# Kernel tuning notes

Hardware: AMD Instinct MI355X
Metric: run time of the kernel (lower is better)

The kernel has to match this reference:

```python
import jax, jax.numpy as jnp
import numpy as np

BETA = 0.01  # soft-threshold level (init kwarg)
EPS = 1e-12


def vector_to_toeplitz(v):
    # v: [2N-1] complex generator; T[i, j] = v[N-1 + i - j], shape [N, N]
    n = (v.shape[0] + 1) // 2
    ii = jnp.arange(n)[:, None]
    jj = jnp.arange(n)[None, :]
    return v[(n - 1) + ii - jj]


def soft_thresh(z, beta):
    # complex soft-threshold (proximal op of beta*||.||_1):
    # z * max(|z| - beta, 0) / |z|
    mag = jnp.abs(z)
    scale = jnp.maximum(mag - beta, 0.0) / jnp.maximum(mag, EPS)
    return z * scale.astype(z.real.dtype)


def setup_inputs() -> dict:
    key = jax.random.key(0)
    ks = jax.random.split(key, 8)
    N, M, B = 1024, 256, 1024
    d = jnp.float32
    return {
        "v_re": jax.random.normal(ks[0], (2 * N - 1,), d),
        "v_im": jax.random.normal(ks[1], (2 * N - 1,), d),
        "W2_re": jax.random.normal(ks[2], (N, M), d) / np.sqrt(M),
        "W2_im": jax.random.normal(ks[3], (N, M), d) / np.sqrt(M),
        "x_re": jax.random.normal(ks[4], (N, B), d),
        "x_im": jax.random.normal(ks[5], (N, B), d),
        "y_re": jax.random.normal(ks[6], (M, B), d),
        "y_im": jax.random.normal(ks[7], (M, B), d),
    }


def reference(v_re, v_im, W2_re, W2_im, x_re, x_im, y_re, y_im):
    v = jax.lax.complex(v_re, v_im)      # [2N-1]
    W2 = jax.lax.complex(W2_re, W2_im)   # [N, M] (= A^H)
    x = jax.lax.complex(x_re, x_im)      # [N, B]
    y = jax.lax.complex(y_re, y_im)      # [M, B]
    W1 = vector_to_toeplitz(v)           # [N, N] Toeplitz
    # tpm(W1, x) + W2 @ y, then complex soft-threshold
    z = soft_thresh(W1 @ x + W2 @ y, BETA)  # [N, B]
    return z
```

## Files before the change

kernel.cpp:

```cpp
#include <hip/hip_runtime.h>
#include <hip/hip_fp16.h>
#include <cstdint>
#include <cstddef>


#define K_DIM 2560
#define BETA_F 0.01f
#define EPS_F  1e-12f

typedef __attribute__((ext_vector_type(8))) _Float16 half8;
typedef __attribute__((ext_vector_type(4))) _Float16 half4;
typedef __attribute__((ext_vector_type(4))) float   floatx4;

__device__ alignas(16) _Float16 g_Ap[1024 * K_DIM];
__device__ alignas(16) _Float16 g_Bt[2048 * K_DIM];
__device__ alignas(16) float    g_P[4][1024 * 2048];

__global__ __launch_bounds__(256) void build_all(
    const float* __restrict__ v_re, const float* __restrict__ v_im,
    const float* __restrict__ W2_re, const float* __restrict__ W2_im,
    const float* __restrict__ x_re, const float* __restrict__ x_im,
    const float* __restrict__ y_re, const float* __restrict__ y_im)
{
    const int bx = blockIdx.x;
    if (bx < 1280) {
        int t = bx * 256 + threadIdx.x;
        int i  = t / 320;
        int c  = t - i * 320;
        int kp = c * 8;
        half8 h;
        if (kp < 1024) {
#pragma unroll
            for (int j = 0; j < 8; ++j) h[j] = (_Float16)v_re[1023 + i - kp - j];
        } else if (kp < 1280) {
            const float* s = W2_re + i * 256 + (kp - 1024);
#pragma unroll
            for (int j = 0; j < 8; ++j) h[j] = (_Float16)s[j];
        } else if (kp < 2304) {
            int k2 = kp - 1280;
#pragma unroll
            for (int j = 0; j < 8; ++j) h[j] = (_Float16)v_im[1023 + i - k2 - j];
        } else {
            const float* s = W2_im + i * 256 + (kp - 2304);
#pragma unroll
            for (int j = 0; j < 8; ++j) h[j] = (_Float16)s[j];
        }
        *reinterpret_cast<half8*>(g_Ap + (size_t)i * K_DIM + kp) = h;
        return;
    }
    __shared__ float lre[32][33];
    __shared__ float lim[32][33];
    int idx = bx - 1280;
    int bk  = idx % 40;
    int by  = idx / 40;
    const float* sre = (bk < 32) ? x_re : y_re;
    const float* sim = (bk < 32) ? x_im : y_im;
    int kb   = (bk < 32) ? bk : (bk - 32);
    int koff = (bk < 32) ? 0 : 1024;
    int k0 = kb * 32;
    int n0 = by * 32;
    int tid = threadIdx.x;
    int tx = tid & 31, ty = tid >> 5;
#pragma unroll
    for (int s = 0; s < 4; ++s) {
        int kk = ty + 8 * s;
        lre[kk][tx] = sre[(size_t)(k0 + kk) * 1024 + n0 + tx];
        lim[kk][tx] = sim[(size_t)(k0 + kk) * 1024 + n0 + tx];
    }
    __syncthreads();
    int lane_n = tid >> 3;
    int kq     = (tid & 7) * 4;
    half4 hre, him, hmim;
#pragma unroll
    for (int j = 0; j < 4; ++j) {
        float re = lre[kq + j][lane_n];
        float im = lim[kq + j][lane_n];
        hre[j]  = (_Float16)re;
        him[j]  = (_Float16)im;
        hmim[j] = (_Float16)(-im);
    }
    int n = n0 + lane_n;
    size_t kk2 = (size_t)koff + k0 + kq;
    _Float16* r0 = g_Bt + (size_t)(2 * n)     * K_DIM;
    _Float16* r1 = g_Bt + (size_t)(2 * n + 1) * K_DIM;
    *reinterpret_cast<half4*>(r0 + kk2)        = hre;
    *reinterpret_cast<half4*>(r0 + kk2 + 1280) = hmim;
    *reinterpret_cast<half4*>(r1 + kk2)        = him;
    *reinterpret_cast<half4*>(r1 + kk2 + 1280) = hre;
}

__global__ __launch_bounds__(256, 8) void gemm_split(void)
{
    __shared__ __align__(16) _Float16 As[2 * 2 * 64 * 32];
    __shared__ __align__(16) _Float16 Bs[2 * 2 * 64 * 32];

    const int tid  = threadIdx.x;
    const int lane = tid & 63;
    const int w    = tid >> 6;
    const int wm   = w >> 1;
    const int wn   = w & 1;

    const int bid   = blockIdx.x;
    const int xcd   = bid & 7;
    const int t     = bid >> 3;
    const int split = t & 3;
    const int tile  = t >> 2;
    const int mi0 = ((xcd & 1) * 8 + (tile & 7)) * 64;
    const int ni0 = ((xcd >> 1) * 8 + (tile >> 3)) * 64;
    const int ks  = split * 640;
    float* __restrict__ P = g_P[split];

    floatx4 acc[2][2];
#pragma unroll
    for (int a = 0; a < 2; ++a)
#pragma unroll
        for (int b = 0; b < 2; ++b) acc[a][b] = (floatx4)0.0f;

    const int rS = tid >> 2;
    const int jS = tid & 3;
    const int s0 = ((rS & 15) >> 1) & 3;
    char* asW = (char*)As + rS * 64 + ((jS ^ s0) * 16);
    char* bsW = (char*)Bs + rS * 64 + ((jS ^ s0) * 16);
    const _Float16* gA = g_Ap + (size_t)(mi0 + rS) * K_DIM + ks + jS * 8;
    const _Float16* gB = g_Bt + (size_t)(ni0 + rS) * K_DIM + ks + jS * 8;

    const int rowA = lane & 15;
    const int q    = lane >> 4;
    const int coff = (q ^ ((rowA >> 1) & 3)) * 16;

    {
        half8 pA0 = *reinterpret_cast<const half8*>(gA);
        half8 pA1 = *reinterpret_cast<const half8*>(gA + 32);
        half8 pB0 = *reinterpret_cast<const half8*>(gB);
        half8 pB1 = *reinterpret_cast<const half8*>(gB + 32);
        *reinterpret_cast<half8*>(asW)        = pA0;
        *reinterpret_cast<half8*>(asW + 4096) = pA1;
        *reinterpret_cast<half8*>(bsW)        = pB0;
        *reinterpret_cast<half8*>(bsW + 4096) = pB1;
    }
    __syncthreads();

    const int NIT = 640 / 64;
    for (int kt = 0; kt < NIT; ++kt) {
        const int cur = kt & 1;
        half8 pA0, pA1, pB0, pB1;
        if (kt < NIT - 1) {
            const _Float16* ga = gA + (kt + 1) * 64;
            const _Float16* gb = gB + (kt + 1) * 64;
            pA0 = *reinterpret_cast<const half8*>(ga);
            pA1 = *reinterpret_cast<const half8*>(ga + 32);
            pB0 = *reinterpret_cast<const half8*>(gb);
            pB1 = *reinterpret_cast<const half8*>(gb + 32);
        }
        const char* Ab = (const char*)As + cur * 8192;
        const char* Bb = (const char*)Bs + cur * 8192;
        half8 af[2][2], bf[2][2];
#pragma unroll
        for (int mi = 0; mi < 2; ++mi) {
            int r = wm * 32 + mi * 16 + rowA;
            af[mi][0] = *reinterpret_cast<const half8*>(Ab + r * 64 + coff);
            af[mi][1] = *reinterpret_cast<const half8*>(Ab + 4096 + r * 64 + coff);
        }
#pragma unroll
        for (int ni = 0; ni < 2; ++ni) {
            int r = wn * 32 + ni * 16 + rowA;
            bf[ni][0] = *reinterpret_cast<const half8*>(Bb + r * 64 + coff);
            bf[ni][1] = *reinterpret_cast<const half8*>(Bb + 4096 + r * 64 + coff);
        }
#pragma unroll
        for (int mi = 0; mi < 2; ++mi)
#pragma unroll
            for (int ni = 0; ni < 2; ++ni) {
                acc[mi][ni] = __builtin_amdgcn_mfma_f32_16x16x32_f16(
                    af[mi][0], bf[ni][0], acc[mi][ni], 0, 0, 0);
                acc[mi][ni] = __builtin_amdgcn_mfma_f32_16x16x32_f16(
                    af[mi][1], bf[ni][1], acc[mi][ni], 0, 0, 0);
            }
        if (kt < NIT - 1) {
            char* aw = asW + (cur ^ 1) * 8192;
            char* bw = bsW + (cur ^ 1) * 8192;
            *reinterpret_cast<half8*>(aw)        = pA0;
            *reinterpret_cast<half8*>(aw + 4096) = pA1;
            *reinterpret_cast<half8*>(bw)        = pB0;
            *reinterpret_cast<half8*>(bw + 4096) = pB1;
        }
        __syncthreads();
    }

    const int colL  = lane & 15;
    const int rquad = (lane >> 4) * 4;
#pragma unroll
    for (int mi = 0; mi < 2; ++mi)
#pragma unroll
        for (int ni = 0; ni < 2; ++ni)
#pragma unroll
            for (int r = 0; r < 4; ++r) {
                int row = mi0 + wm * 32 + mi * 16 + rquad + r;
                int col = ni0 + wn * 32 + ni * 16 + colL;
                P[(size_t)row * 2048 + col] = acc[mi][ni][r];
            }
}

__global__ __launch_bounds__(256) void reduce_soft(float* __restrict__ out,
                                                   int out_n)
{
    int t = blockIdx.x * 256 + threadIdx.x;
    floatx4 v0 = reinterpret_cast<const floatx4*>(g_P[0])[t];
    floatx4 v1 = reinterpret_cast<const floatx4*>(g_P[1])[t];
    floatx4 v2 = reinterpret_cast<const floatx4*>(g_P[2])[t];
    floatx4 v3 = reinterpret_cast<const floatx4*>(g_P[3])[t];
    float re0 = (v0[0] + v1[0]) + (v2[0] + v3[0]);
    float im0 = (v0[1] + v1[1]) + (v2[1] + v3[1]);
    float re1 = (v0[2] + v1[2]) + (v2[2] + v3[2]);
    float im1 = (v0[3] + v1[3]) + (v2[3] + v3[3]);
    float m0 = sqrtf(re0 * re0 + im0 * im0);
    float m1 = sqrtf(re1 * re1 + im1 * im1);
    float s0 = fmaxf(m0 - BETA_F, 0.0f) / fmaxf(m0, EPS_F);
    float s1 = fmaxf(m1 - BETA_F, 0.0f) / fmaxf(m1, EPS_F);
    float2 r = make_float2(re0 * s0, re1 * s1);
    int idx = t * 2;
    if (idx + 1 < out_n)
        *reinterpret_cast<float2*>(out + idx) = r;
}

extern "C" void kernel_launch(void* const* d_in, const int* in_sizes, int n_in,
                              void* d_out, int out_size, void* d_ws, size_t ws_size,
                              hipStream_t stream) {
    (void)d_ws; (void)ws_size; (void)in_sizes; (void)n_in;
    const float* v_re  = (const float*)d_in[0];
    const float* v_im  = (const float*)d_in[1];
    const float* W2_re = (const float*)d_in[2];
    const float* W2_im = (const float*)d_in[3];
    const float* x_re  = (const float*)d_in[4];
    const float* x_im  = (const float*)d_in[5];
    const float* y_re  = (const float*)d_in[6];
    const float* y_im  = (const float*)d_in[7];
    float* out = (float*)d_out;

    build_all<<<2560, 256, 0, stream>>>(v_re, v_im, W2_re, W2_im,
                                        x_re, x_im, y_re, y_im);
    gemm_split<<<2048, 256, 0, stream>>>();
    reduce_soft<<<2048, 256, 0, stream>>>(out, out_size);
}
```

Measured before the change: 122.6 us.

## Fuse split-K reduction and soft-threshold into GEMM via last-arriver atomic counter

Split-K drops from four slices to two, and the separate reduce kernel is removed. The second block to finish a tile, found through an atomic counter, adds the other slice's partial from global memory and applies the complex soft-threshold in place, exchanging real and imaginary parts with a lane shuffle. This cuts partial-buffer traffic and one kernel launch. In exchange the grid is smaller and each block runs longer, and threadfence plus atomics add synchronisation. Every block still writes its partials, and the out writes are strided, scalar and only use half the lanes.

```diff
diff --git a/kernel.cpp b/kernel.cpp
--- a/kernel.cpp
+++ b/kernel.cpp
@@ -14,7 +14,8 @@
 
 __device__ alignas(16) _Float16 g_Ap[1024 * K_DIM];
 __device__ alignas(16) _Float16 g_Bt[2048 * K_DIM];
-__device__ alignas(16) float    g_P[4][1024 * 2048];
+__device__ alignas(16) float    g_P[2][1024 * 2048];
+__device__ int g_cnt[512];
 
 __global__ __launch_bounds__(256) void build_all(
     const float* __restrict__ v_re, const float* __restrict__ v_im,
@@ -25,6 +26,7 @@
     const int bx = blockIdx.x;
     if (bx < 1280) {
         int t = bx * 256 + threadIdx.x;
+        if (t < 512) g_cnt[t] = 0;
         int i  = t / 320;
         int c  = t - i * 320;
         int kp = c * 8;
@@ -89,10 +91,12 @@
     *reinterpret_cast<half4*>(r1 + kk2 + 1280) = hre;
 }
 
-__global__ __launch_bounds__(256, 8) void gemm_split(void)
+__global__ __launch_bounds__(256, 4) void gemm_fused(float* __restrict__ out,
+                                                     int out_n)
 {
     __shared__ __align__(16) _Float16 As[2 * 2 * 64 * 32];
     __shared__ __align__(16) _Float16 Bs[2 * 2 * 64 * 32];
+    __shared__ int sLast;
 
     const int tid  = threadIdx.x;
     const int lane = tid & 63;
@@ -100,14 +104,14 @@
     const int wm   = w >> 1;
     const int wn   = w & 1;
 
-    const int bid   = blockIdx.x;
-    const int xcd   = bid & 7;
-    const int t     = bid >> 3;
-    const int split = t & 3;
-    const int tile  = t >> 2;
-    const int mi0 = ((xcd & 1) * 8 + (tile & 7)) * 64;
-    const int ni0 = ((xcd >> 1) * 8 + (tile >> 3)) * 64;
-    const int ks  = split * 640;
+    const int bid    = blockIdx.x;
+    const int split  = (bid >> 3) & 1;
+    const int tileId = (bid & 7) | ((bid >> 4) << 3);
+    const int xcd    = tileId & 7;
+    const int t      = tileId >> 3;
+    const int mi0 = ((xcd & 1) * 8 + (t & 7)) * 64;
+    const int ni0 = ((xcd >> 1) * 8 + (t >> 3)) * 64;
+    const int ks  = split * 1280;
     float* __restrict__ P = g_P[split];
 
     floatx4 acc[2][2];
@@ -140,7 +144,7 @@
     }
     __syncthreads();
 
-    const int NIT = 640 / 64;
+    const int NIT = 1280 / 64;
     for (int kt = 0; kt < NIT; ++kt) {
         const int cur = kt & 1;
         half8 pA0, pA1, pB0, pB1;
@@ -199,28 +203,32 @@
                 int col = ni0 + wn * 32 + ni * 16 + colL;
                 P[(size_t)row * 2048 + col] = acc[mi][ni][r];
             }
-}
-
-__global__ __launch_bounds__(256) void reduce_soft(float* __restrict__ out,
-                                                   int out_n)
-{
-    int t = blockIdx.x * 256 + threadIdx.x;
-    floatx4 v0 = reinterpret_cast<const floatx4*>(g_P[0])[t];
-    floatx4 v1 = reinterpret_cast<const floatx4*>(g_P[1])[t];
-    floatx4 v2 = reinterpret_cast<const floatx4*>(g_P[2])[t];
-    floatx4 v3 = reinterpret_cast<const floatx4*>(g_P[3])[t];
-    float re0 = (v0[0] + v1[0]) + (v2[0] + v3[0]);
-    float im0 = (v0[1] + v1[1]) + (v2[1] + v3[1]);
-    float re1 = (v0[2] + v1[2]) + (v2[2] + v3[2]);
-    float im1 = (v0[3] + v1[3]) + (v2[3] + v3[3]);
-    float m0 = sqrtf(re0 * re0 + im0 * im0);
-    float m1 = sqrtf(re1 * re1 + im1 * im1);
-    float s0 = fmaxf(m0 - BETA_F, 0.0f) / fmaxf(m0, EPS_F);
-    float s1 = fmaxf(m1 - BETA_F, 0.0f) / fmaxf(m1, EPS_F);
-    float2 r = make_float2(re0 * s0, re1 * s1);
-    int idx = t * 2;
-    if (idx + 1 < out_n)
-        *reinterpret_cast<float2*>(out + idx) = r;
+    __threadfence();
+    __syncthreads();
+    if (tid == 0)
+        sLast = (atomicAdd(&g_cnt[tileId], 1) == 1);
+    __syncthreads();
+    if (!sLast) return;
+
+    __threadfence();
+    const float* __restrict__ O = g_P[split ^ 1];
+#pragma unroll
+    for (int mi = 0; mi < 2; ++mi)
+#pragma unroll
+        for (int ni = 0; ni < 2; ++ni)
+#pragma unroll
+            for (int r = 0; r < 4; ++r) {
+                int row = mi0 + wm * 32 + mi * 16 + rquad + r;
+                int col = ni0 + wn * 32 + ni * 16 + colL;
+                float c = acc[mi][ni][r] + O[(size_t)row * 2048 + col];
+                float p = __shfl_xor(c, 1, 64);
+                float mag = sqrtf(c * c + p * p);
+                float s = fmaxf(mag - BETA_F, 0.0f) / fmaxf(mag, EPS_F);
+                if ((col & 1) == 0) {
+                    size_t idx = (size_t)row * 1024 + (col >> 1);
+                    if (idx < (size_t)out_n) out[idx] = c * s;
+                }
+            }
 }
 
 extern "C" void kernel_launch(void* const* d_in, const int* in_sizes, int n_in,
@@ -239,6 +247,5 @@
 
     build_all<<<2560, 256, 0, stream>>>(v_re, v_im, W2_re, W2_im,
                                         x_re, x_im, y_re, y_im);
-    gemm_split<<<2048, 256, 0, stream>>>();
-    reduce_soft<<<2048, 256, 0, stream>>>(out, out_size);
+    gemm_fused<<<1024, 256, 0, stream>>>(out, out_size);
 }
```

After: 318.4 us. 2.6x slower.

## Halve split-K factor and add two-stage register prefetch in GEMM

Applied to the files above, without the earlier changes.

Cuts the split-K factor from 4 to 2, so each block walks 1280 K elements and only two partial buffers are written and read by the reduction. This removes a large share of the fp32 partial-sum traffic. The main loop now prefetches global tiles two iterations ahead into rotating registers, and the occupancy hint is relaxed to 4 to make room for them. In exchange the grid is half as large, which leaves less parallelism and longer per-block latency.

```diff
diff --git a/kernel.cpp b/kernel.cpp
--- a/kernel.cpp
+++ b/kernel.cpp
@@ -14,7 +14,7 @@
 
 __device__ alignas(16) _Float16 g_Ap[1024 * K_DIM];
 __device__ alignas(16) _Float16 g_Bt[2048 * K_DIM];
-__device__ alignas(16) float    g_P[4][1024 * 2048];
+__device__ alignas(16) float    g_P[2][1024 * 2048];
 
 __global__ __launch_bounds__(256) void build_all(
     const float* __restrict__ v_re, const float* __restrict__ v_im,
@@ -89,7 +89,7 @@
     *reinterpret_cast<half4*>(r1 + kk2 + 1280) = hre;
 }
 
-__global__ __launch_bounds__(256, 8) void gemm_split(void)
+__global__ __launch_bounds__(256, 4) void gemm_split(void)
 {
     __shared__ __align__(16) _Float16 As[2 * 2 * 64 * 32];
     __shared__ __align__(16) _Float16 Bs[2 * 2 * 64 * 32];
@@ -101,13 +101,13 @@
     const int wn   = w & 1;
 
     const int bid   = blockIdx.x;
-    const int xcd   = bid & 7;
-    const int t     = bid >> 3;
-    const int split = t & 3;
-    const int tile  = t >> 2;
-    const int mi0 = ((xcd & 1) * 8 + (tile & 7)) * 64;
-    const int ni0 = ((xcd >> 1) * 8 + (tile >> 3)) * 64;
-    const int ks  = split * 640;
+    const int split = bid >> 9;
+    const int sb    = bid & 511;
+    const int xcd   = sb & 7;
+    const int t     = sb >> 3;
+    const int mi0 = ((xcd & 1) * 8 + (t & 7)) * 64;
+    const int ni0 = ((xcd >> 1) * 8 + (t >> 3)) * 64;
+    const int ks  = split * 1280;
     float* __restrict__ P = g_P[split];
 
     floatx4 acc[2][2];
@@ -128,29 +128,37 @@
     const int q    = lane >> 4;
     const int coff = (q ^ ((rowA >> 1) & 3)) * 16;
 
+    const int NIT = 1280 / 64;
+
+    half8 sA0[2], sA1[2], sB0[2], sB1[2];
+
     {
-        half8 pA0 = *reinterpret_cast<const half8*>(gA);
-        half8 pA1 = *reinterpret_cast<const half8*>(gA + 32);
-        half8 pB0 = *reinterpret_cast<const half8*>(gB);
-        half8 pB1 = *reinterpret_cast<const half8*>(gB + 32);
-        *reinterpret_cast<half8*>(asW)        = pA0;
-        *reinterpret_cast<half8*>(asW + 4096) = pA1;
-        *reinterpret_cast<half8*>(bsW)        = pB0;
-        *reinterpret_cast<half8*>(bsW + 4096) = pB1;
+        half8 a0 = *reinterpret_cast<const half8*>(gA);
+        half8 a1 = *reinterpret_cast<const half8*>(gA + 32);
+        half8 b0 = *reinterpret_cast<const half8*>(gB);
+        half8 b1 = *reinterpret_cast<const half8*>(gB + 32);
+        sA0[1] = *reinterpret_cast<const half8*>(gA + 64);
+        sA1[1] = *reinterpret_cast<const half8*>(gA + 96);
+        sB0[1] = *reinterpret_cast<const half8*>(gB + 64);
+        sB1[1] = *reinterpret_cast<const half8*>(gB + 96);
+        *reinterpret_cast<half8*>(asW)        = a0;
+        *reinterpret_cast<half8*>(asW + 4096) = a1;
+        *reinterpret_cast<half8*>(bsW)        = b0;
+        *reinterpret_cast<half8*>(bsW + 4096) = b1;
     }
     __syncthreads();
 
-    const int NIT = 640 / 64;
+#pragma unroll 2
     for (int kt = 0; kt < NIT; ++kt) {
         const int cur = kt & 1;
-        half8 pA0, pA1, pB0, pB1;
-        if (kt < NIT - 1) {
-            const _Float16* ga = gA + (kt + 1) * 64;
-            const _Float16* gb = gB + (kt + 1) * 64;
-            pA0 = *reinterpret_cast<const half8*>(ga);
-            pA1 = *reinterpret_cast<const half8*>(ga + 32);
-            pB0 = *reinterpret_cast<const half8*>(gb);
-            pB1 = *reinterpret_cast<const half8*>(gb + 32);
+        const int nxt = cur ^ 1;
+        if (kt + 2 < NIT) {
+            const _Float16* ga = gA + (size_t)(kt + 2) * 64;
+            const _Float16* gb = gB + (size_t)(kt + 2) * 64;
+            sA0[cur] = *reinterpret_cast<const half8*>(ga);
+            sA1[cur] = *reinterpret_cast<const half8*>(ga + 32);
+            sB0[cur] = *reinterpret_cast<const half8*>(gb);
+            sB1[cur] = *reinterpret_cast<const half8*>(gb + 32);
         }
         const char* Ab = (const char*)As + cur * 8192;
         const char* Bb = (const char*)Bs + cur * 8192;
@@ -176,13 +184,13 @@
                 acc[mi][ni] = __builtin_amdgcn_mfma_f32_16x16x32_f16(
                     af[mi][1], bf[ni][1], acc[mi][ni], 0, 0, 0);
             }
-        if (kt < NIT - 1) {
-            char* aw = asW + (cur ^ 1) * 8192;
-            char* bw = bsW + (cur ^ 1) * 8192;
-            *reinterpret_cast<half8*>(aw)        = pA0;
-            *reinterpret_cast<half8*>(aw + 4096) = pA1;
-            *reinterpret_cast<half8*>(bw)        = pB0;
-            *reinterpret_cast<half8*>(bw + 4096) = pB1;
+        if (kt + 1 < NIT) {
+            char* aw = asW + nxt * 8192;
+            char* bw = bsW + nxt * 8192;
+            *reinterpret_cast<half8*>(aw)        = sA0[nxt];
+            *reinterpret_cast<half8*>(aw + 4096) = sA1[nxt];
+            *reinterpret_cast<half8*>(bw)        = sB0[nxt];
+            *reinterpret_cast<half8*>(bw + 4096) = sB1[nxt];
         }
         __syncthreads();
     }
@@ -207,12 +215,8 @@
     int t = blockIdx.x * 256 + threadIdx.x;
     floatx4 v0 = reinterpret_cast<const floatx4*>(g_P[0])[t];
     floatx4 v1 = reinterpret_cast<const floatx4*>(g_P[1])[t];
-    floatx4 v2 = reinterpret_cast<const floatx4*>(g_P[2])[t];
-    floatx4 v3 = reinterpret_cast<const floatx4*>(g_P[3])[t];
-    float re0 = (v0[0] + v1[0]) + (v2[0] + v3[0]);
-    float im0 = (v0[1] + v1[1]) + (v2[1] + v3[1]);
-    float re1 = (v0[2] + v1[2]) + (v2[2] + v3[2]);
-    float im1 = (v0[3] + v1[3]) + (v2[3] + v3[3]);
+    float re0 = v0[0] + v1[0], im0 = v0[1] + v1[1];
+    float re1 = v0[2] + v1[2], im1 = v0[3] + v1[3];
     float m0 = sqrtf(re0 * re0 + im0 * im0);
     float m1 = sqrtf(re1 * re1 + im1 * im1);
     float s0 = fmaxf(m0 - BETA_F, 0.0f) / fmaxf(m0, EPS_F);
@@ -239,6 +243,6 @@
 
     build_all<<<2560, 256, 0, stream>>>(v_re, v_im, W2_re, W2_im,
                                         x_re, x_im, y_re, y_im);
-    gemm_split<<<2048, 256, 0, stream>>>();
+    gemm_split<<<1024, 256, 0, stream>>>();
     reduce_soft<<<2048, 256, 0, stream>>>(out, out_size);
 }
```

Result: faster. 115.2 us (-6.0%).
